# Performance work log

Hardware: AMD Instinct MI355X
Metric: run time of the kernel (lower is better)

Reference implementation:

```python
import jax, jax.numpy as jnp
import numpy as np

N_TOK = 256
C_Z = 128
C = 32
N_HEAD = 4


def setup_inputs() -> dict:
    key = jax.random.key(0)
    ks = jax.random.split(key, 8)
    s = 0.02
    return {
        "z": jax.random.normal(ks[0], (N_TOK, N_TOK, C_Z), dtype=jnp.float32),
        "single_mask": jnp.ones((N_TOK,), dtype=jnp.float32),
        "ln_gamma": jnp.ones((C_Z,), dtype=jnp.float32),
        "ln_beta": jnp.zeros((C_Z,), dtype=jnp.float32),
        "W_q": jax.random.normal(ks[1], (C_Z, N_HEAD * C), dtype=jnp.float32) * s,
        "W_k": jax.random.normal(ks[2], (C_Z, N_HEAD * C), dtype=jnp.float32) * s,
        "W_v": jax.random.normal(ks[3], (C_Z, N_HEAD * C), dtype=jnp.float32) * s,
        "W_b": jax.random.normal(ks[4], (C_Z, N_HEAD), dtype=jnp.float32) * s,
        "W_g": jax.random.normal(ks[5], (C_Z, N_HEAD * C), dtype=jnp.float32) * s,
        "W_out": jax.random.normal(ks[6], (N_HEAD * C, C_Z), dtype=jnp.float32) * s,
    }


def reference(z, single_mask, ln_gamma, ln_beta, W_q, W_k, W_v, W_b, W_g, W_out):
    # LayerNorm over c_z
    mu = jnp.mean(z, axis=-1, keepdims=True)
    var = jnp.var(z, axis=-1, keepdims=True)
    zn = (z - mu) * jax.lax.rsqrt(var + 1e-5) * ln_gamma + ln_beta

    n = zn.shape[0]
    proj = lambda W: (zn @ W).reshape(n, n, N_HEAD, C)
    q = proj(W_q)
    k = proj(W_k)
    v = proj(W_v)
    g = proj(W_g)
    b = zn @ W_b  # [i, j, h] -> used as bias b[j, k, h]

    # a[i,j,k,h] = q[i,j]·k[i,k]/sqrt(c) + b[j,k,h]
    a = jnp.einsum('ijhc,ikhc->ijkh', q, k) / np.sqrt(C).astype(np.float32)
    a = a + b[None, :, :, :]
    a = a + (-1e9) * (1.0 - single_mask)[None, None, :, None]
    a = jax.nn.softmax(a, axis=-2)  # over k

    o = jnp.einsum('ijkh,ikhc->ijhc', a, v)
    o = jax.nn.sigmoid(g) * o
    o = o.reshape(n, n, N_HEAD * C)
    return o @ W_out
```

## Files before the change

kernel.cpp:

```cpp
#include <hip/hip_runtime.h>
#include <hip/hip_bf16.h>

#define NT 256
#define CZ 128
#define CH 32
#define NH 4
#define PL 2097152

typedef unsigned short ushort_t;
typedef unsigned int uint_t;
typedef __attribute__((ext_vector_type(8))) short short8;
typedef __attribute__((ext_vector_type(4))) float f32x4;

__device__ __forceinline__ float bfbits2f(uint_t bits){
  union { uint_t u; float f; } v; v.u = bits; return v.f;
}
__device__ __forceinline__ float bf2f(ushort_t u){
  return bfbits2f(((uint_t)u) << 16);
}
__device__ __forceinline__ ushort_t f2bf(float f){
  union { float f; uint_t u; } v; v.f = f;
  uint_t u = v.u;
  uint_t r = (u + 0x7fffu + ((u >> 16) & 1u)) >> 16;
  return (ushort_t)r;
}
__device__ __forceinline__ void unpk(uint_t w, float& lo, float& hi){
  lo = bfbits2f(w << 16);
  hi = bfbits2f(w & 0xffff0000u);
}
__device__ __forceinline__ short8 as_s8(uint4 u){
  union { uint4 u; short8 s; } v; v.u = u; return v.s;
}
__device__ __forceinline__ int detect_f32(const ushort_t* zz){
  int l = threadIdx.x & 63;
  int bad = 0;
  #pragma unroll
  for(int s=0;s<4;s++){
    float v = bf2f(zz[l*4 + s]);
    if(!(fabsf(v) < 1e9f)) bad = 1;
  }
  return (__ballot(bad) != 0ull) ? 1 : 0;
}

__global__ void k_cvt_small(const void* __restrict__ m_, const void* __restrict__ g_,
    const void* __restrict__ b_, const void* __restrict__ wb_,
    float* __restrict__ dst, const ushort_t* __restrict__ zz){
  int isf32 = detect_f32(zz);
  int idx = threadIdx.x * 4;
  const void* sp; int off;
  if(idx < 256){ sp = m_;  off = idx; }
  else if(idx < 384){ sp = g_;  off = idx-256; }
  else if(idx < 512){ sp = b_;  off = idx-384; }
  else { sp = wb_; off = idx-512; }
  float4 o;
  if(isf32){ o = *(const float4*)((const float*)sp + off); }
  else {
    uint2 u = *(const uint2*)((const ushort_t*)sp + off);
    unpk(u.x, o.x, o.y); unpk(u.y, o.z, o.w);
  }
  *(float4*)(dst + idx) = o;
}

__global__ __launch_bounds__(256) void k_cvt_wt(const void* __restrict__ s0,
    const void* __restrict__ s1, const void* __restrict__ s2,
    const void* __restrict__ s3, const void* __restrict__ s4,
    ushort_t* __restrict__ dst, const ushort_t* __restrict__ zz){
  int isf32 = detect_f32(zz);
  const void* srcs[5] = {s0,s1,s2,s3,s4};
  int w = blockIdx.x >> 6;
  int idx = (blockIdx.x & 63)*256 + threadIdx.x;
  int k = idx >> 7, c = idx & 127;
  const void* sp = srcs[w];
  float v;
  if(isf32) v = ((const float*)sp)[idx];
  else      v = bf2f(((const ushort_t*)sp)[idx]);
  dst[(size_t)w*16384 + (size_t)c*128 + k] = f2bf(v);
}

__global__ __launch_bounds__(256) void k_lnproj(const void* __restrict__ zraw,
    const float* __restrict__ smallf, const ushort_t* __restrict__ Wt,
    ushort_t* __restrict__ qh, ushort_t* __restrict__ kh,
    ushort_t* __restrict__ vh, ushort_t* __restrict__ gh,
    float* __restrict__ btm){
  __shared__ __align__(16) char lds[47104];
  ushort_t* znl = (ushort_t*)lds;
  float*    tbB = (float*)(lds + 34816);
  float*    wbs = (float*)(lds + 45056);
  const float* mkf = smallf;
  const float* gmf = smallf + 256;
  const float* btf = smallf + 384;
  const float* Wbf = smallf + 512;
  int t = threadIdx.x;
  int isf32 = detect_f32((const ushort_t*)zraw);
  wbs[t] = Wbf[t]; wbs[t+256] = Wbf[t+256];
  __syncthreads();

  int row_loc = t >> 1, half = t & 1;
  size_t r = (size_t)blockIdx.x*128 + row_loc;
  float mval = -1e9f * (1.f - mkf[r & 255]);
  float s = 0.f, s2 = 0.f;
  if(isf32){
    const float4* zp = (const float4*)((const float*)zraw + r*CZ + half*64);
    #pragma unroll
    for(int q=0;q<16;q++){
      float4 v = zp[q];
      s  += (v.x + v.y) + (v.z + v.w);
      s2 += (v.x*v.x + v.y*v.y) + (v.z*v.z + v.w*v.w);
    }
  } else {
    const uint4* zp = (const uint4*)((const ushort_t*)zraw + r*CZ + half*64);
    #pragma unroll
    for(int q=0;q<8;q++){
      uint4 u = zp[q];
      const uint_t* pu = (const uint_t*)&u;
      #pragma unroll
      for(int e=0;e<4;e++){
        float lo, hi; unpk(pu[e], lo, hi);
        s += lo + hi; s2 += lo*lo + hi*hi;
      }
    }
  }
  s  += __shfl_xor(s, 1);
  s2 += __shfl_xor(s2, 1);
  float mu  = s * (1.f/CZ);
  float var = fmaxf(s2 * (1.f/CZ) - mu*mu, 0.f);
  float rs  = rsqrtf(var + 1e-5f);
  float acch[4] = {0.f,0.f,0.f,0.f};
  #pragma unroll
  for(int chunk=0;chunk<8;chunk++){
    float v8[8];
    if(isf32){
      const float4* zp = (const float4*)((const float*)zraw + r*CZ + half*64 + chunk*8);
      float4 a = zp[0], b = zp[1];
      v8[0]=a.x; v8[1]=a.y; v8[2]=a.z; v8[3]=a.w;
      v8[4]=b.x; v8[5]=b.y; v8[6]=b.z; v8[7]=b.w;
    } else {
      uint4 u = *(const uint4*)((const ushort_t*)zraw + r*CZ + half*64 + chunk*8);
      const uint_t* pu = (const uint_t*)&u;
      #pragma unroll
      for(int e=0;e<4;e++) unpk(pu[e], v8[e*2], v8[e*2+1]);
    }
    uint_t ow[4];
    #pragma unroll
    for(int e2=0;e2<4;e2++){
      int cg = half*64 + chunk*8 + e2*2;
      float v0 = (v8[e2*2]   - mu)*rs*gmf[cg]   + btf[cg];
      float v1 = (v8[e2*2+1] - mu)*rs*gmf[cg+1] + btf[cg+1];
      float4 w0 = *(const float4*)&wbs[cg*4];
      float4 w1 = *(const float4*)&wbs[(cg+1)*4];
      acch[0] += v0*w0.x + v1*w1.x;
      acch[1] += v0*w0.y + v1*w1.y;
      acch[2] += v0*w0.z + v1*w1.z;
      acch[3] += v0*w0.w + v1*w1.w;
      ow[e2] = (uint_t)f2bf(v0) | ((uint_t)f2bf(v1) << 16);
    }
    uint4 o; o.x=ow[0]; o.y=ow[1]; o.z=ow[2]; o.w=ow[3];
    *(uint4*)(znl + row_loc*136 + half*64 + chunk*8) = o;
  }
  #pragma unroll
  for(int h=0;h<4;h++){
    float tot = acch[h] + __shfl_xor(acch[h], 1);
    if(half == 0) btm[(size_t)h*65536 + r] = (tot + mval) * 1.4426950408889634f;
  }
  __syncthreads();

  int wave = t>>6, l = t&63, n = l&15, quad = l>>4;
  uint4 af[2][4];
  #pragma unroll
  for(int mt=0;mt<2;mt++)
    #pragma unroll
    for(int kb=0;kb<4;kb++)
      af[mt][kb] = *(const uint4*)(znl + (wave*32 + mt*16 + n)*136 + kb*32 + quad*8);
  float* T = tbB + wave*640;
  int rrow = l >> 1, rhalf = l & 1;
  ushort_t* outs[4] = {qh, kh, vh, gh};
  size_t row0 = (size_t)blockIdx.x*128 + wave*32;
  #pragma unroll
  for(int w=0;w<4;w++){
    const ushort_t* W = Wt + (size_t)w*16384;
    ushort_t* D = outs[w];
    float sc = (w==0) ? (0.17677669529663687f * 1.4426950408889634f) : 1.f;
    #pragma unroll
    for(int nt=0;nt<8;nt++){
      uint4 bfr[4];
      #pragma unroll
      for(int kb=0;kb<4;kb++)
        bfr[kb] = *(const uint4*)(W + ((size_t)(nt*16 + n))*128 + kb*32 + quad*8);
      f32x4 a0 = {0.f,0.f,0.f,0.f}, a1 = {0.f,0.f,0.f,0.f};
      #pragma unroll
      for(int kb=0;kb<4;kb++){
        a0 = __builtin_amdgcn_mfma_f32_16x16x32_bf16(as_s8(af[0][kb]), as_s8(bfr[kb]), a0, 0,0,0);
        a1 = __builtin_amdgcn_mfma_f32_16x16x32_bf16(as_s8(af[1][kb]), as_s8(bfr[kb]), a1, 0,0,0);
      }
      #pragma unroll
      for(int rr=0;rr<4;rr++){
        T[(quad*4 + rr)*20 + n]      = a0[rr];
        T[(16 + quad*4 + rr)*20 + n] = a1[rr];
      }
      float4 v0 = *(const float4*)(T + rrow*20 + rhalf*8);
      float4 v1 = *(const float4*)(T + rrow*20 + rhalf*8 + 4);
      uint4 o;
      o.x = (uint_t)f2bf(v0.x*sc) | ((uint_t)f2bf(v0.y*sc) << 16);
      o.y = (uint_t)f2bf(v0.z*sc) | ((uint_t)f2bf(v0.w*sc) << 16);
      o.z = (uint_t)f2bf(v1.x*sc) | ((uint_t)f2bf(v1.y*sc) << 16);
      o.w = (uint_t)f2bf(v1.z*sc) | ((uint_t)f2bf(v1.w*sc) << 16);
      *(uint4*)(D + (size_t)(nt>>1)*PL + (row0 + rrow)*CH + (nt&1)*16 + rhalf*8) = o;
    }
  }
}

__global__ __launch_bounds__(256, 4) void k_attn(
    const ushort_t* __restrict__ qh, const ushort_t* __restrict__ kh,
    const ushort_t* __restrict__ vh, const ushort_t* __restrict__ gh,
    const float* __restrict__ btm, ushort_t* __restrict__ oh){
  __shared__ __align__(16) char lds[40960];
  uint4*    VfA = (uint4*)lds;
  ushort_t* Pw0 = (ushort_t*)(lds + 16384);
  uint4*    Kf  = (uint4*)(lds + 24576);
  ushort_t* Vn  = (ushort_t*)(lds + 16384);
  int t = threadIdx.x;
  int i = blockIdx.x >> 2, h = blockIdx.x & 3;
  int wave = t >> 6, l = t & 63;
  int n = l & 15, quad = l >> 4;
  const ushort_t* qhp = qh + (size_t)h*PL + (size_t)(i*NT)*CH;
  const ushort_t* khp = kh + (size_t)h*PL + (size_t)(i*NT)*CH;
  const ushort_t* vhp = vh + (size_t)h*PL + (size_t)(i*NT)*CH;
  const ushort_t* ghp = gh + (size_t)h*PL + (size_t)(i*NT)*CH;
  ushort_t*       ohp = oh + (size_t)h*PL + (size_t)(i*NT)*CH;
  const float*    bth = btm + (size_t)h*65536;

  uint4 kreg[4];
  #pragma unroll
  for(int m=0;m<4;m++)
    kreg[m] = *(const uint4*)(khp + (size_t)((wave*4+m)*16 + n)*CH + quad*8);

  {
    const uint4* vp = (const uint4*)(vhp + t*CH);
    uint4 u0=vp[0], u1=vp[1], u2=vp[2], u3=vp[3];
    uint4* dstp = (uint4*)(Vn + t*40);
    dstp[0]=u0; dstp[1]=u1; dstp[2]=u2; dstp[3]=u3;
  }
  __syncthreads();
  {
    #pragma unroll
    for(int it=0; it<4; it++){
      int u = wave + it*4, kblk = u >> 1, ct = u & 1;
      uint_t d[4];
      #pragma unroll
      for(int e=0;e<4;e++){
        uint_t lo = Vn[(kblk*32 + quad*8 + e*2    )*40 + ct*16 + n];
        uint_t hi = Vn[(kblk*32 + quad*8 + e*2 + 1)*40 + ct*16 + n];
        d[e] = lo | (hi << 16);
      }
      uint4 o; o.x=d[0]; o.y=d[1]; o.z=d[2]; o.w=d[3];
      VfA[u*64 + l] = o;
    }
  }
  __syncthreads();
  {
    #pragma unroll
    for(int m=0;m<4;m++) Kf[(wave*4+m)*64 + l] = kreg[m];
  }
  __syncthreads();

  ushort_t* Pw = Pw0 + wave*1024;
  int swz = (n & 7) << 4;

  for(int s=0;s<4;s++){
    int jt = wave*4 + s;
    uint4 qf = *(const uint4*)(qhp + (size_t)(jt*16 + n)*CH + quad*8);
    const float* brow = bth + (size_t)(jt*16 + n)*256 + quad*4;
    f32x4 oa0 = {0.f,0.f,0.f,0.f}, oa1 = {0.f,0.f,0.f,0.f};
    float sum0 = 0.f, sum1 = 0.f;
    #pragma unroll
    for(int Q=0;Q<4;Q++){
      f32x4 acc[4];
      #pragma unroll
      for(int m=0;m<4;m++)
        acc[m] = *(const f32x4*)(brow + (Q*4+m)*16);
      #pragma unroll
      for(int m=0;m<4;m++){
        uint4 kfv = Kf[(Q*4+m)*64 + l];
        acc[m] = __builtin_amdgcn_mfma_f32_16x16x32_bf16(as_s8(kfv), as_s8(qf), acc[m], 0,0,0);
      }
      #pragma unroll
      for(int m=0;m<4;m++){
        float e0 = exp2f(acc[m][0]);
        float e1 = exp2f(acc[m][1]);
        float e2 = exp2f(acc[m][2]);
        float e3 = exp2f(acc[m][3]);
        sum0 += e0 + e1; sum1 += e2 + e3;
        uint2 pv;
        pv.x = (uint_t)f2bf(e0) | ((uint_t)f2bf(e1) << 16);
        pv.y = (uint_t)f2bf(e2) | ((uint_t)f2bf(e3) << 16);
        *(uint2*)((char*)Pw + (((n<<7) + (m<<5) + (quad<<3)) ^ swz)) = pv;
      }
      #pragma unroll
      for(int kb=0;kb<2;kb++){
        uint4 pf = *(const uint4*)((char*)Pw + (((n<<7) + (kb<<6) + (quad<<4)) ^ swz));
        int kg = Q*2 + kb;
        oa0 = __builtin_amdgcn_mfma_f32_16x16x32_bf16(as_s8(VfA[(kg*2+0)*64 + l]), as_s8(pf), oa0, 0,0,0);
        oa1 = __builtin_amdgcn_mfma_f32_16x16x32_bf16(as_s8(VfA[(kg*2+1)*64 + l]), as_s8(pf), oa1, 0,0,0);
      }
    }
    float ssum = sum0 + sum1;
    ssum += __shfl_xor(ssum, 16);
    ssum += __shfl_xor(ssum, 32);
    float inv = 1.f / ssum;
    size_t rb = (size_t)(jt*16 + n)*CH;
    uint2 g0 = *(const uint2*)(ghp + rb + quad*4);
    uint2 g1 = *(const uint2*)(ghp + rb + 16 + quad*4);
    float ga[4], gc[4];
    unpk(g0.x, ga[0], ga[1]); unpk(g0.y, ga[2], ga[3]);
    unpk(g1.x, gc[0], gc[1]); unpk(g1.y, gc[2], gc[3]);
    float v0[4], v1[4];
    #pragma unroll
    for(int rr=0;rr<4;rr++){
      v0[rr] = oa0[rr] * inv * (1.f/(1.f + __expf(-ga[rr])));
      v1[rr] = oa1[rr] * inv * (1.f/(1.f + __expf(-gc[rr])));
    }
    uint2 s0, s1;
    s0.x = (uint_t)f2bf(v0[0]) | ((uint_t)f2bf(v0[1]) << 16);
    s0.y = (uint_t)f2bf(v0[2]) | ((uint_t)f2bf(v0[3]) << 16);
    s1.x = (uint_t)f2bf(v1[0]) | ((uint_t)f2bf(v1[1]) << 16);
    s1.y = (uint_t)f2bf(v1[2]) | ((uint_t)f2bf(v1[3]) << 16);
    *(uint2*)(ohp + rb + quad*4)      = s0;
    *(uint2*)(ohp + rb + 16 + quad*4) = s1;
  }
}

__global__ __launch_bounds__(256) void k_gemm1(const ushort_t* __restrict__ oh,
    const ushort_t* __restrict__ Wt, void* __restrict__ outp,
    const ushort_t* __restrict__ zz){
  __shared__ __align__(16) float tbB[4*640];
  int isf32 = detect_f32(zz);
  int t = threadIdx.x, wave = t>>6, l = t&63, n = l&15, quad = l>>4;
  size_t row0 = (size_t)blockIdx.x*128 + wave*32;
  float* T = tbB + wave*640;
  int rrow = l >> 1, rhalf = l & 1;
  uint4 af[2][4];
  #pragma unroll
  for(int mt=0;mt<2;mt++)
    #pragma unroll
    for(int kb=0;kb<4;kb++)
      af[mt][kb] = *(const uint4*)(oh + (size_t)kb*PL + (row0 + mt*16 + n)*CH + quad*8);
  #pragma unroll
  for(int nt=0;nt<8;nt++){
    uint4 bfr[4];
    #pragma unroll
    for(int kb=0;kb<4;kb++)
      bfr[kb] = *(const uint4*)(Wt + ((size_t)(nt*16 + n))*128 + kb*32 + quad*8);
    f32x4 a0 = {0.f,0.f,0.f,0.f}, a1 = {0.f,0.f,0.f,0.f};
    #pragma unroll
    for(int kb=0;kb<4;kb++){
      a0 = __builtin_amdgcn_mfma_f32_16x16x32_bf16(as_s8(af[0][kb]), as_s8(bfr[kb]), a0, 0,0,0);
      a1 = __builtin_amdgcn_mfma_f32_16x16x32_bf16(as_s8(af[1][kb]), as_s8(bfr[kb]), a1, 0,0,0);
    }
    #pragma unroll
    for(int rr=0;rr<4;rr++){
      T[(quad*4 + rr)*20 + n]      = a0[rr];
      T[(16 + quad*4 + rr)*20 + n] = a1[rr];
    }
    float4 v0 = *(const float4*)(T + rrow*20 + rhalf*8);
    float4 v1 = *(const float4*)(T + rrow*20 + rhalf*8 + 4);
    if(isf32){
      float* of = (float*)outp + (row0 + rrow)*CZ + nt*16 + rhalf*8;
      *(float4*)of = v0;
      *(float4*)(of + 4) = v1;
    } else {
      uint4 o;
      o.x = (uint_t)f2bf(v0.x) | ((uint_t)f2bf(v0.y) << 16);
      o.y = (uint_t)f2bf(v0.z) | ((uint_t)f2bf(v0.w) << 16);
      o.z = (uint_t)f2bf(v1.x) | ((uint_t)f2bf(v1.y) << 16);
      o.w = (uint_t)f2bf(v1.z) | ((uint_t)f2bf(v1.w) << 16);
      *(uint4*)((ushort_t*)outp + (row0 + rrow)*CZ + nt*16 + rhalf*8) = o;
    }
  }
}

extern "C" void kernel_launch(void* const* d_in, const int* in_sizes, int n_in,
                              void* d_out, int out_size, void* d_ws, size_t ws_size,
                              hipStream_t stream){
  char* wsb = (char*)d_ws;
  const size_t TB = (size_t)16777216;
  ushort_t* qh  = (ushort_t*)(wsb);
  ushort_t* kh  = (ushort_t*)(wsb + TB);
  ushort_t* vh  = (ushort_t*)(wsb + 2*TB);
  ushort_t* gh  = (ushort_t*)(wsb + 3*TB);
  ushort_t* oh  = (ushort_t*)(wsb + 4*TB);
  float*    btm = (float*)   (wsb + 5*TB);
  float*  smallf= (float*)   (wsb + 5*TB + (1u<<20));
  ushort_t* Wt  = (ushort_t*)(wsb + 5*TB + (1u<<20) + 4096);
  const ushort_t* zz = (const ushort_t*)d_in[0];

  k_cvt_small<<<1,   256, 0, stream>>>(d_in[1], d_in[2], d_in[3], d_in[7], smallf, zz);
  k_cvt_wt   <<<320, 256, 0, stream>>>(d_in[4], d_in[5], d_in[6], d_in[8], d_in[9], Wt, zz);
  k_lnproj   <<<512, 256, 0, stream>>>(d_in[0], smallf, Wt, qh, kh, vh, gh, btm);
  k_attn     <<<1024,256, 0, stream>>>(qh, kh, vh, gh, btm, oh);
  k_gemm1    <<<512, 256, 0, stream>>>(oh, Wt + (size_t)4*16384, d_out, zz);
}
```

Before: 225.4 us.

## Restructure attention prologue, prefetch Q/gate rows, use native exp2 and bf16 pack

Rewrites the k_attn prologue so K fragments go straight from global memory into LDS and V fragments are gathered directly from global memory, instead of staging V through a padded LDS buffer. This drops one barrier and gives K, V and P their own LDS regions. Q and gate values for all four row tiles are now loaded up front, so their latency overlaps with compute, and the loop over tiles is fully unrolled. It also switches to the hardware exp2 builtin and the library bf16 conversion, and removes the occupancy hint from the launch bounds. The trade-offs are strided 2-byte global gathers for V and higher register pressure.

Result: slower. 230.5 us (+2.3%).

```diff
diff --git a/kernel.cpp b/kernel.cpp
--- a/kernel.cpp
+++ b/kernel.cpp
@@ -30,6 +30,11 @@
 }
 __device__ __forceinline__ short8 as_s8(uint4 u){
   union { uint4 u; short8 s; } v; v.u = u; return v.s;
+}
+__device__ __forceinline__ uint_t pk2(float a, float b){
+  union { __hip_bfloat16 h; ushort_t u; } x, y;
+  x.h = __float2bfloat16(a); y.h = __float2bfloat16(b);
+  return (uint_t)x.u | ((uint_t)y.u << 16);
 }
 __device__ __forceinline__ int detect_f32(const ushort_t* zz){
   int l = threadIdx.x & 63;
@@ -209,15 +214,14 @@
   }
 }
 
-__global__ __launch_bounds__(256, 4) void k_attn(
+__global__ __launch_bounds__(256) void k_attn(
     const ushort_t* __restrict__ qh, const ushort_t* __restrict__ kh,
     const ushort_t* __restrict__ vh, const ushort_t* __restrict__ gh,
     const float* __restrict__ btm, ushort_t* __restrict__ oh){
   __shared__ __align__(16) char lds[40960];
   uint4*    VfA = (uint4*)lds;
-  ushort_t* Pw0 = (ushort_t*)(lds + 16384);
-  uint4*    Kf  = (uint4*)(lds + 24576);
-  ushort_t* Vn  = (ushort_t*)(lds + 16384);
+  uint4*    Kf  = (uint4*)(lds + 16384);
+  ushort_t* Pw0 = (ushort_t*)(lds + 32768);
   int t = threadIdx.x;
   int i = blockIdx.x >> 2, h = blockIdx.x & 3;
   int wave = t >> 6, l = t & 63;
@@ -229,18 +233,13 @@
   ushort_t*       ohp = oh + (size_t)h*PL + (size_t)(i*NT)*CH;
   const float*    bth = btm + (size_t)h*65536;
 
-  uint4 kreg[4];
-  #pragma unroll
-  for(int m=0;m<4;m++)
-    kreg[m] = *(const uint4*)(khp + (size_t)((wave*4+m)*16 + n)*CH + quad*8);
-
   {
-    const uint4* vp = (const uint4*)(vhp + t*CH);
-    uint4 u0=vp[0], u1=vp[1], u2=vp[2], u3=vp[3];
-    uint4* dstp = (uint4*)(Vn + t*40);
-    dstp[0]=u0; dstp[1]=u1; dstp[2]=u2; dstp[3]=u3;
-  }
-  __syncthreads();
+    #pragma unroll
+    for(int m=0;m<4;m++){
+      int kt = wave*4 + m;
+      Kf[kt*64 + l] = *(const uint4*)(khp + (size_t)(kt*16 + n)*CH + quad*8);
+    }
+  }
   {
     #pragma unroll
     for(int it=0; it<4; it++){
@@ -248,8 +247,8 @@
       uint_t d[4];
       #pragma unroll
       for(int e=0;e<4;e++){
-        uint_t lo = Vn[(kblk*32 + quad*8 + e*2    )*40 + ct*16 + n];
-        uint_t hi = Vn[(kblk*32 + quad*8 + e*2 + 1)*40 + ct*16 + n];
+        uint_t lo = vhp[(size_t)(kblk*32 + quad*8 + e*2    )*CH + ct*16 + n];
+        uint_t hi = vhp[(size_t)(kblk*32 + quad*8 + e*2 + 1)*CH + ct*16 + n];
         d[e] = lo | (hi << 16);
       }
       uint4 o; o.x=d[0]; o.y=d[1]; o.z=d[2]; o.w=d[3];
@@ -257,18 +256,24 @@
     }
   }
   __syncthreads();
-  {
-    #pragma unroll
-    for(int m=0;m<4;m++) Kf[(wave*4+m)*64 + l] = kreg[m];
-  }
-  __syncthreads();
 
   ushort_t* Pw = Pw0 + wave*1024;
   int swz = (n & 7) << 4;
 
+  uint4 qf[4];
+  uint2 gp0[4], gp1[4];
+  #pragma unroll
   for(int s=0;s<4;s++){
     int jt = wave*4 + s;
-    uint4 qf = *(const uint4*)(qhp + (size_t)(jt*16 + n)*CH + quad*8);
+    size_t rb = (size_t)(jt*16 + n)*CH;
+    qf[s]  = *(const uint4*)(qhp + rb + quad*8);
+    gp0[s] = *(const uint2*)(ghp + rb + quad*4);
+    gp1[s] = *(const uint2*)(ghp + rb + 16 + quad*4);
+  }
+
+  #pragma unroll
+  for(int s=0;s<4;s++){
+    int jt = wave*4 + s;
     const float* brow = bth + (size_t)(jt*16 + n)*256 + quad*4;
     f32x4 oa0 = {0.f,0.f,0.f,0.f}, oa1 = {0.f,0.f,0.f,0.f};
     float sum0 = 0.f, sum1 = 0.f;
@@ -281,18 +286,18 @@
       #pragma unroll
       for(int m=0;m<4;m++){
         uint4 kfv = Kf[(Q*4+m)*64 + l];
-        acc[m] = __builtin_amdgcn_mfma_f32_16x16x32_bf16(as_s8(kfv), as_s8(qf), acc[m], 0,0,0);
+        acc[m] = __builtin_amdgcn_mfma_f32_16x16x32_bf16(as_s8(kfv), as_s8(qf[s]), acc[m], 0,0,0);
       }
       #pragma unroll
       for(int m=0;m<4;m++){
-        float e0 = exp2f(acc[m][0]);
-        float e1 = exp2f(acc[m][1]);
-        float e2 = exp2f(acc[m][2]);
-        float e3 = exp2f(acc[m][3]);
+        float e0 = __builtin_amdgcn_exp2f(acc[m][0]);
+        float e1 = __builtin_amdgcn_exp2f(acc[m][1]);
+        float e2 = __builtin_amdgcn_exp2f(acc[m][2]);
+        float e3 = __builtin_amdgcn_exp2f(acc[m][3]);
         sum0 += e0 + e1; sum1 += e2 + e3;
         uint2 pv;
-        pv.x = (uint_t)f2bf(e0) | ((uint_t)f2bf(e1) << 16);
-        pv.y = (uint_t)f2bf(e2) | ((uint_t)f2bf(e3) << 16);
+        pv.x = pk2(e0, e1);
+        pv.y = pk2(e2, e3);
         *(uint2*)((char*)Pw + (((n<<7) + (m<<5) + (quad<<3)) ^ swz)) = pv;
       }
       #pragma unroll
@@ -308,11 +313,9 @@
     ssum += __shfl_xor(ssum, 32);
     float inv = 1.f / ssum;
     size_t rb = (size_t)(jt*16 + n)*CH;
-    uint2 g0 = *(const uint2*)(ghp + rb + quad*4);
-    uint2 g1 = *(const uint2*)(ghp + rb + 16 + quad*4);
     float ga[4], gc[4];
-    unpk(g0.x, ga[0], ga[1]); unpk(g0.y, ga[2], ga[3]);
-    unpk(g1.x, gc[0], gc[1]); unpk(g1.y, gc[2], gc[3]);
+    unpk(gp0[s].x, ga[0], ga[1]); unpk(gp0[s].y, ga[2], ga[3]);
+    unpk(gp1[s].x, gc[0], gc[1]); unpk(gp1[s].y, gc[2], gc[3]);
     float v0[4], v1[4];
     #pragma unroll
     for(int rr=0;rr<4;rr++){
```
